# Optimization experiments

Measured on AMD Instinct MI355X. Metric: run time of the kernel, lower is better.

## Reference

```python
import jax, jax.numpy as jnp
import numpy as np

B, T, P, H, E, K, COND = 4096, 20, 20, 256, 128, 5, 5
CTX = E + H + P  # embedded condition + encoder hidden + time-stamp one-hot-cumsum


def setup_inputs():
    key = jax.random.key(0)
    ks = jax.random.split(key, 12)
    g = lambda k, sh, s=0.05: (jax.random.normal(k, sh) * s).astype(jnp.float32)
    return dict(
        conditions=g(ks[0], (B, T, COND), 1.0),
        state_h=g(ks[1], (B, H), 0.1),
        state_c=g(ks[2], (B, H), 0.1),
        steps_n=T,
        We1=g(ks[3], (COND, E)), be1=jnp.zeros((E,), jnp.float32),
        We2=g(ks[4], (E, E)), be2=jnp.zeros((E,), jnp.float32),
        Wk=g(ks[5], (CTX, 4 * H)), Wr=g(ks[6], (H, 4 * H)), bl=jnp.zeros((4 * H,), jnp.float32),
        Wm=g(ks[7], (H, 6 * K)), bm=jnp.zeros((6 * K,), jnp.float32),
        Wy=g(ks[8], (H, 3 * K)), by=jnp.zeros((3 * K,), jnp.float32),
        Wf=g(ks[9], (H, 3 * K)), bf=jnp.zeros((3 * K,), jnp.float32),
        Wfadj=g(ks[10], (H, 3 * K)), bfadj=jnp.zeros((3 * K,), jnp.float32),
    )


def _decode(conditions, state_h, state_c, steps_n, We1, be1, We2, be2,
            Wk, Wr, bl, Wm, bm, Wy, by, Wf, bf, Wfadj, bfadj):
    Bn = conditions.shape[0]
    enc_h = state_h  # reshaped encoder hidden, concatenated into context every step
    base_key = jax.random.key(42)

    def lstm_step(x):
        # Keras gate order i,f,c,o. NOTE: original resets initial_state=self.state
        # (never updated) so every step starts from the encoder state -- kept faithful.
        z = x @ Wk + state_h @ Wr + bl
        i, f, g, o = jnp.split(z, 4, axis=-1)
        c = jax.nn.sigmoid(f) * state_c + jax.nn.sigmoid(i) * jnp.tanh(g)
        return jax.nn.sigmoid(o) * jnp.tanh(c)

    def head_other(h, W, b, k):
        # univariate GMM head: [softmax alphas | mus | exp sigmas], plus one sample
        p = h @ W + b
        logits, mu, ls = jnp.split(p, 3, axis=-1)
        alphas, sig = jax.nn.softmax(logits, axis=-1), jnp.exp(ls)
        vec = jnp.concatenate([alphas, mu, sig], axis=-1)
        k1, k2 = jax.random.split(k)
        idx = jax.random.categorical(k1, logits)[:, None]
        mu_k = jnp.take_along_axis(mu, idx, 1)
        s_k = jnp.take_along_axis(sig, idx, 1)
        return vec, mu_k + s_k * jax.random.normal(k2, mu_k.shape)

    def step(carry, i):
        cond, key = carry
        key, km, ky, kf, kfa = jax.random.split(key, 5)
        emb = (cond @ We1 + be1) @ We2 + be2  # fc_embedding: two linear Dense layers
        ts = (jnp.arange(P) <= i).astype(cond.dtype)  # cumulative time stamp (faithful)
        ctx = jnp.concatenate([emb, enc_h, jnp.broadcast_to(ts, (Bn, P))], axis=-1)
        h = lstm_step(ctx)
        # merge vehicle: bivariate correlated GMM
        pm = h @ Wm + bm
        logits, mu_lo, ls_lo, mu_la, ls_la, rr = jnp.split(pm, 6, axis=-1)
        alphas = jax.nn.softmax(logits, axis=-1)
        s_lo, s_la, rho = jnp.exp(ls_lo), jnp.exp(ls_la), jnp.tanh(rr)
        vec_m = jnp.concatenate([alphas, mu_lo, s_lo, mu_la, s_la, rho], axis=-1)
        k1, k2 = jax.random.split(km)
        idx = jax.random.categorical(k1, logits)[:, None]
        take = lambda a: jnp.take_along_axis(a, idx, 1)
        z = jax.random.normal(k2, (Bn, 2))
        x_lo = take(mu_lo) + take(s_lo) * z[:, :1]
        r = take(rho)
        x_la = take(mu_la) + take(s_la) * (r * z[:, :1] + jnp.sqrt(1.0 - r * r) * z[:, 1:])
        vec_y, s_y = head_other(h, Wy, by, ky)
        vec_f, s_f = head_other(h, Wf, bf, kf)
        vec_fa, s_fa = head_other(h, Wfadj, bfadj, kfa)
        new_cond = jnp.concatenate([x_lo, x_la, s_y, s_f, s_fa], axis=-1)  # [B,5]
        return (new_cond, key), (vec_m, vec_y, vec_f, vec_fa)

    init = (conditions[:, 0, :], base_key)
    _, (vm, vy, vf, vfa) = jax.lax.scan(step, init, jnp.arange(steps_n))
    tr = lambda a: jnp.transpose(a, (1, 0, 2))  # [T,B,D] -> [B,T,D]
    return tr(vm), tr(vy), tr(vf), tr(vfa)


def reference(conditions, state_h, state_c, steps_n, We1, be1, We2, be2,
              Wk, Wr, bl, Wm, bm, Wy, by, Wf, bf, Wfadj, bfadj):
    # returns the concatenated GMM parameter sequences for (merge, yield, f, fadj)
    return _decode(conditions, state_h, state_c, steps_n, We1, be1, We2, be2,
                   Wk, Wr, bl, Wm, bm, Wy, by, Wf, bf, Wfadj, bfadj)
```

## Files before the change

kernel.cpp:

```cpp
#include <hip/hip_runtime.h>
#include <stdint.h>
#include <math.h>

#define BN 4096
#define TT 20
#define HH 256
#define EE 128
#define KK 5
#define NCOND 5

#define WS_TSC  512
#define WS_WTB  20992
#define WS_BIAS 41472
#define WS_ZC   42320
#define WS_M    43344
#define WS_WSUM 48464
#define WS_G    310608
#define WS_ZM   (WS_G + 4*TT*BN*KK)
#define WS_ZO   (WS_ZM + TT*BN*2)
#define WS_CZ   (WS_ZO + 3*TT*BN)
#define WS_END  (WS_CZ + BN*1024)

#define PSTR 84

#define TINYF 1.17549435e-38f
#define LO_N  0.99999994f
#define LOG2E 1.44269504f
#define LN2   0.69314718f

typedef __attribute__((ext_vector_type(8))) short short8v;
typedef __attribute__((ext_vector_type(4))) float f32x4;

__device__ __host__ __forceinline__ constexpr void tf2(
    uint32_t k0, uint32_t k1, uint32_t x0, uint32_t x1, uint32_t& o0, uint32_t& o1) {
  const uint32_t ks2 = k0 ^ k1 ^ 0x1BD11BDAu;
  x0 += k0; x1 += k1;
#define RND(r) { x0 += x1; x1 = (x1 << (r)) | (x1 >> (32 - (r))); x1 ^= x0; }
  RND(13) RND(15) RND(26) RND(6)   x0 += k1;  x1 += ks2 + 1u;
  RND(17) RND(29) RND(16) RND(24)  x0 += ks2; x1 += k0 + 2u;
  RND(13) RND(15) RND(26) RND(6)   x0 += k0;  x1 += k1 + 3u;
  RND(17) RND(29) RND(16) RND(24)  x0 += k1;  x1 += ks2 + 4u;
  RND(13) RND(15) RND(26) RND(6)   x0 += ks2; x1 += k0 + 5u;
#undef RND
  o0 = x0; o1 = x1;
}

struct KeyTab { uint32_t v[TT * 16]; };
constexpr KeyTab mkkeys() {
  KeyTab kt{};
  uint32_t kx = 0u, ky = 42u;
  for (int t = 0; t < TT; ++t) {
    for (int l = 0; l < 4; ++l) {
      uint32_t hx = 0, hy = 0, a = 0, b = 0, c = 0, d = 0;
      tf2(kx, ky, 0u, (uint32_t)(l + 1), hx, hy);
      tf2(hx, hy, 0u, 0u, a, b);
      tf2(hx, hy, 0u, 1u, c, d);
      kt.v[t * 16 + l * 4 + 0] = a;
      kt.v[t * 16 + l * 4 + 1] = b;
      kt.v[t * 16 + l * 4 + 2] = c;
      kt.v[t * 16 + l * 4 + 3] = d;
    }
    uint32_t nx = 0, ny = 0;
    tf2(kx, ky, 0u, 0u, nx, ny);
    kx = nx; ky = ny;
  }
  return kt;
}
__constant__ KeyTab KT = mkkeys();

__device__ __forceinline__ uint32_t pbits(uint32_t k0, uint32_t k1, uint32_t n) {
  uint32_t a, b;
  tf2(k0, k1, 0u, n, a, b);
  return a ^ b;
}

__device__ __forceinline__ float u01f(uint32_t bits) {
  return __uint_as_float((bits >> 9) | 0x3f800000u) - 1.0f;
}

__device__ __forceinline__ float fexp(float x) { return __builtin_amdgcn_exp2f(x * LOG2E); }
__device__ __forceinline__ float flog(float x) { return __builtin_amdgcn_logf(x) * LN2; }
__device__ __forceinline__ float frcp(float x) { return __builtin_amdgcn_rcpf(x); }
__device__ __forceinline__ float fsig(float x) {
  return frcp(1.0f + __builtin_amdgcn_exp2f(-x * LOG2E));
}
__device__ __forceinline__ float ftanh(float x) {
  return 1.0f - 2.0f * frcp(1.0f + __builtin_amdgcn_exp2f(x * (2.0f * LOG2E)));
}

__device__ __forceinline__ float erfinv_f(float x) {
  float w = -flog(fmaf(-x, x, 1.0f));
  float p;
  if (w < 5.0f) {
    w = w - 2.5f;
    p = 2.81022636e-08f;
    p = 3.43273939e-07f + p * w;
    p = -3.5233877e-06f + p * w;
    p = -4.39150654e-06f + p * w;
    p = 0.00021858087f  + p * w;
    p = -0.00125372503f + p * w;
    p = -0.00417768164f + p * w;
    p = 0.246640727f    + p * w;
    p = 1.50140941f     + p * w;
  } else {
    w = sqrtf(w) - 3.0f;
    p = -0.000200214257f;
    p = 0.000100950558f + p * w;
    p = 0.00134934322f  + p * w;
    p = -0.00367342844f + p * w;
    p = 0.00573950773f  + p * w;
    p = -0.0076224613f  + p * w;
    p = 0.00943887047f  + p * w;
    p = 1.00167406f     + p * w;
    p = 2.83297682f     + p * w;
  }
  return p * x;
}

__device__ __forceinline__ uint32_t bf16rne(float f) {
  uint32_t u = __float_as_uint(f);
  return (u + 0x7fffu + ((u >> 16) & 1u)) >> 16;
}

#define RB_RNG   0
#define RB_WSUM  8000
#define RB_TSC   9024
#define RB_WTB   9028
#define RB_BIAS  9108
#define RB_MZC   9109
#define RB_TOT   9113
__global__ __launch_bounds__(256) void prep_misc(
    const float* __restrict__ Wk, const float* __restrict__ Wr,
    const float* __restrict__ We1, const float* __restrict__ be1,
    const float* __restrict__ We2, const float* __restrict__ be2,
    const float* __restrict__ Wm, const float* __restrict__ bm,
    const float* __restrict__ Wy, const float* __restrict__ by,
    const float* __restrict__ Wf, const float* __restrict__ bf,
    const float* __restrict__ Wfa, const float* __restrict__ bfa,
    const float* __restrict__ bl, float* __restrict__ ws) {
  __shared__ float smem[768];
  const int bid = blockIdx.x, tid = threadIdx.x;

  if (bid < RB_WSUM) {
    const int id = bid * 256 + tid;
    const int NG = 4 * TT * BN * KK;
    if (id < NG) {
      const int t = id / (BN * 4 * KK);
      const int r1 = id % (BN * 4 * KK);
      const int row = r1 / (4 * KK);
      const int r2 = r1 % (4 * KK);
      const int head = r2 / KK, k = r2 % KK;
      const uint32_t k0 = KT.v[t * 16 + head * 4 + 0], k1 = KT.v[t * 16 + head * 4 + 1];
      float u = u01f(pbits(k0, k1, (uint32_t)(row * KK + k)));
      u = fmaxf(TINYF, u * (1.0f - TINYF) + TINYF);
      ws[WS_G + id] = -flog(-flog(u));
    } else if (id < NG + TT * BN * 2) {
      const int jj = id - NG;
      const int t = jj / (BN * 2);
      const uint32_t n = (uint32_t)(jj % (BN * 2));
      const uint32_t k0 = KT.v[t * 16 + 2], k1 = KT.v[t * 16 + 3];
      float u = u01f(pbits(k0, k1, n)) * 2.0f - LO_N;
      u = fmaxf(-LO_N, u);
      ws[WS_ZM + jj] = 1.41421356f * erfinv_f(u);
    } else {
      const int jj = id - NG - TT * BN * 2;
      const int t = jj / (BN * 3);
      const int r2 = jj % (BN * 3);
      const int row = r2 / 3, hh = r2 % 3;
      const uint32_t k0 = KT.v[t * 16 + (hh + 1) * 4 + 2];
      const uint32_t k1 = KT.v[t * 16 + (hh + 1) * 4 + 3];
      float u = u01f(pbits(k0, k1, (uint32_t)row)) * 2.0f - LO_N;
      u = fmaxf(-LO_N, u);
      ws[WS_ZO + jj] = 1.41421356f * erfinv_f(u);
    }
  } else if (bid < RB_TSC) {
    const int idx = (bid - RB_WSUM) * 256 + tid;
    const int q = idx >> 10, col = idx & 1023;
    ws[WS_WSUM + idx] = Wk[(size_t)(EE + q) * 1024 + col] + Wr[(size_t)q * 1024 + col];
  } else if (bid < RB_WTB) {
    const int col = (bid - RB_TSC) * 256 + tid;
    float s = 0.0f;
    for (int p = 0; p < TT; ++p) {
      s += Wk[(size_t)(EE + HH + p) * 1024 + col];
      ws[WS_TSC + p * 1024 + col] = s;
    }
  } else if (bid < RB_BIAS) {
    const int idx = (bid - RB_WTB) * 256 + tid;
    const int o = idx >> 8, q = idx & 255;
    float v = 0.0f;
    if (o < 30)      v = Wm[q * 30 + o];
    else if (o < 45) v = Wy[q * 15 + (o - 30)];
    else if (o < 60) v = Wf[q * 15 + (o - 45)];
    else if (o < 75) v = Wfa[q * 15 + (o - 60)];
    uint16_t* wtb = (uint16_t*)&ws[WS_WTB];
    wtb[o * 256 + (q ^ ((o & 7) << 3))] = (uint16_t)bf16rne(v);
  } else if (bid == RB_BIAS) {
    if (tid < 80) {
      float v = 0.0f;
      if (tid < 30)      v = bm[tid];
      else if (tid < 45) v = by[tid - 30];
      else if (tid < 60) v = bf[tid - 45];
      else if (tid < 75) v = bfa[tid - 60];
      ws[WS_BIAS + tid] = v;
    }
  } else {
    float* T1s = smem;
    float* eb2s = smem + 640;
    if (tid < EE) {
      const int q = tid;
      float t0 = 0.f, t1 = 0.f, t2 = 0.f, t3 = 0.f, t4 = 0.f;
      float eb = be2[q];
      for (int e = 0; e < EE; ++e) {
        const float w2 = We2[e * EE + q];
        t0 = fmaf(We1[0 * EE + e], w2, t0);
        t1 = fmaf(We1[1 * EE + e], w2, t1);
        t2 = fmaf(We1[2 * EE + e], w2, t2);
        t3 = fmaf(We1[3 * EE + e], w2, t3);
        t4 = fmaf(We1[4 * EE + e], w2, t4);
        eb = fmaf(be1[e], w2, eb);
      }
      T1s[0 * 128 + q] = t0; T1s[1 * 128 + q] = t1; T1s[2 * 128 + q] = t2;
      T1s[3 * 128 + q] = t3; T1s[4 * 128 + q] = t4; eb2s[q] = eb;
    }
    __syncthreads();
    const int col = (bid - RB_MZC) * 256 + tid;
    float m0 = 0.f, m1 = 0.f, m2 = 0.f, m3 = 0.f, m4 = 0.f;
    float zacc = bl[col];
    for (int q = 0; q < EE; ++q) {
      const float wv = Wk[(size_t)q * 1024 + col];
      m0 = fmaf(T1s[0 * 128 + q], wv, m0);
      m1 = fmaf(T1s[1 * 128 + q], wv, m1);
      m2 = fmaf(T1s[2 * 128 + q], wv, m2);
      m3 = fmaf(T1s[3 * 128 + q], wv, m3);
      m4 = fmaf(T1s[4 * 128 + q], wv, m4);
      zacc = fmaf(eb2s[q], wv, zacc);
    }
    ws[WS_M + 0 * 1024 + col] = m0;
    ws[WS_M + 1 * 1024 + col] = m1;
    ws[WS_M + 2 * 1024 + col] = m2;
    ws[WS_M + 3 * 1024 + col] = m3;
    ws[WS_M + 4 * 1024 + col] = m4;
    ws[WS_ZC + col] = zacc;
  }
}

__global__ __launch_bounds__(512) void prep_czgemm(
    const float* __restrict__ state_h, float* __restrict__ ws) {
  __shared__ short Ab[128 * 256];
  __shared__ short Bb[128 * 256];
  const int tid = threadIdx.x;
  const int brow = blockIdx.x >> 3, bcol = blockIdx.x & 7;
  const int row0 = brow * 128, col0 = bcol * 128;

  for (int i = tid; i < 128 * 256; i += 512) {
    const int m = i >> 8, k = i & 255;
    Ab[m * 256 + (k ^ ((m & 7) << 3))] =
        (short)bf16rne(state_h[(size_t)(row0 + m) * HH + k]);
  }
  for (int i = tid; i < 128 * 256; i += 512) {
    const int k = i >> 7, n = i & 127;
    Bb[n * 256 + (k ^ ((n & 7) << 3))] =
        (short)bf16rne(ws[WS_WSUM + k * 1024 + col0 + n]);
  }
  __syncthreads();

  const int wv = tid >> 6, lane = tid & 63;
  const int wr = wv >> 2, wc = wv & 3;
  const int rc = lane & 15, hq = lane >> 4;
  f32x4 acc[4][2];
#pragma unroll
  for (int fr = 0; fr < 4; ++fr)
#pragma unroll
    for (int fc = 0; fc < 2; ++fc) acc[fr][fc] = (f32x4){0.f, 0.f, 0.f, 0.f};

#pragma unroll
  for (int kk = 0; kk < 8; ++kk) {
    const int kbase = kk * 32 + hq * 8;
    short8v av[4], bv[2];
#pragma unroll
    for (int fr = 0; fr < 4; ++fr) {
      const int m = wr * 64 + fr * 16 + rc;
      av[fr] = *(const short8v*)&Ab[m * 256 + (kbase ^ ((m & 7) << 3))];
    }
#pragma unroll
    for (int fc = 0; fc < 2; ++fc) {
      const int n = wc * 32 + fc * 16 + rc;
      bv[fc] = *(const short8v*)&Bb[n * 256 + (kbase ^ ((n & 7) << 3))];
    }
#pragma unroll
    for (int fr = 0; fr < 4; ++fr)
#pragma unroll
      for (int fc = 0; fc < 2; ++fc)
        acc[fr][fc] = __builtin_amdgcn_mfma_f32_16x16x32_bf16(av[fr], bv[fc],
                                                              acc[fr][fc], 0, 0, 0);
  }

#pragma unroll
  for (int fc = 0; fc < 2; ++fc) {
    const int colg = col0 + wc * 32 + fc * 16 + rc;
    const float zcv = ws[WS_ZC + colg];
#pragma unroll
    for (int fr = 0; fr < 4; ++fr) {
#pragma unroll
      for (int j = 0; j < 4; ++j) {
        const int row = row0 + wr * 64 + fr * 16 + hq * 4 + j;
        ws[WS_CZ + (size_t)row * 1024 + colg] = acc[fr][fc][j] + zcv;
      }
    }
  }
}

__global__ __launch_bounds__(512) void decode_main(
    const float* __restrict__ conditions, const float* __restrict__ state_h,
    const float* __restrict__ state_c, const float* __restrict__ ws,
    float* __restrict__ out, int use_cz) {
  __shared__ float Msh[5 * 1024];
  __shared__ short WTBs[80 * 256];
  __shared__ short hb[16 * 256];
  __shared__ float psh[8 * PSTR];
  __shared__ float biasL[80];
  __shared__ float conds[8 * 8];

  const int tid = threadIdx.x;
  const int row0 = blockIdx.x * 8;
  const int u = tid & 255;
  const int half = tid >> 8;
  const int rbase = half * 4;

  for (int i = tid; i < 5 * 1024; i += 512) Msh[i] = ws[WS_M + i];
  if (tid < 80) biasL[tid] = ws[WS_BIAS + tid];
  if (tid < 8 * NCOND) {
    const int r = tid / NCOND, c = tid - r * NCOND;
    conds[r * 8 + c] = conditions[(size_t)(row0 + r) * (TT * NCOND) + c];
  }
  float sc[4];
#pragma unroll
  for (int rr = 0; rr < 4; ++rr) sc[rr] = state_c[(size_t)(row0 + rbase + rr) * HH + u];

  const bool cth = (tid < 256);
  const int kci = tid & 7;
  const int rci = tid >> 5;
  const int headci = (tid >> 3) & 3;
  const int crow = row0 + rci;
  const int cbase2 = headci ? (30 + 15 * (headci - 1)) : 0;

  float cz[4][4];
  if (use_cz) {
#pragma unroll
    for (int g = 0; g < 4; ++g)
#pragma unroll
      for (int rr = 0; rr < 4; ++rr)
        cz[g][rr] = ws[WS_CZ + (size_t)(row0 + rbase + rr) * 1024 + g * 256 + u];
    {
      uint32_t* dst = (uint32_t*)WTBs;
      const uint32_t* src = (const uint32_t*)&ws[WS_WTB];
      for (int i = tid; i < 80 * 128; i += 512) dst[i] = src[i];
      uint32_t* hz = (uint32_t*)hb;
      for (int i = tid; i < 1024; i += 512) hz[1024 + i] = 0u;
    }
    __syncthreads();
  } else {
    float* hstage = (float*)WTBs;
    for (int i = tid; i < 8 * HH; i += 512) hstage[i] = state_h[(size_t)row0 * HH + i];
    __syncthreads();
#pragma unroll
    for (int g = 0; g < 4; ++g) {
      const float z = ws[WS_ZC + g * 256 + u];
#pragma unroll
      for (int rr = 0; rr < 4; ++rr) cz[g][rr] = z;
    }
    for (int q = 0; q < HH; ++q) {
      const float w0 = ws[WS_WSUM + q * 1024 + u];
      const float w1 = ws[WS_WSUM + q * 1024 + 256 + u];
      const float w2 = ws[WS_WSUM + q * 1024 + 512 + u];
      const float w3 = ws[WS_WSUM + q * 1024 + 768 + u];
#pragma unroll
      for (int rr = 0; rr < 4; ++rr) {
        const float e = hstage[(rbase + rr) * HH + q];
        cz[0][rr] = fmaf(e, w0, cz[0][rr]);
        cz[1][rr] = fmaf(e, w1, cz[1][rr]);
        cz[2][rr] = fmaf(e, w2, cz[2][rr]);
        cz[3][rr] = fmaf(e, w3, cz[3][rr]);
      }
    }
    __syncthreads();
    {
      uint32_t* dst = (uint32_t*)WTBs;
      const uint32_t* src = (const uint32_t*)&ws[WS_WTB];
      for (int i = tid; i < 80 * 128; i += 512) dst[i] = src[i];
      uint32_t* hz = (uint32_t*)hb;
      for (int i = tid; i < 1024; i += 512) hz[1024 + i] = 0u;
    }
    __syncthreads();
  }

  for (int t = 0; t < TT; ++t) {
    float pg = 0.0f, pz0 = 0.0f, pz1 = 0.0f, pzz = 0.0f;
    if (cth) {
      if (kci < 5)
        pg = ws[WS_G + (((size_t)t * BN + crow) * 4 + headci) * KK + kci];
      if (kci == 0) {
        if (headci == 0) {
          pz0 = ws[WS_ZM + ((size_t)t * BN + crow) * 2 + 0];
          pz1 = ws[WS_ZM + ((size_t)t * BN + crow) * 2 + 1];
        } else {
          pzz = ws[WS_ZO + ((size_t)t * BN + crow) * 3 + (headci - 1)];
        }
      }
    }
    {
      const float ts0 = ws[WS_TSC + t * 1024 + u];
      const float ts1 = ws[WS_TSC + t * 1024 + 256 + u];
      const float ts2 = ws[WS_TSC + t * 1024 + 512 + u];
      const float ts3 = ws[WS_TSC + t * 1024 + 768 + u];
      float mA[5], mB[5], mC[5], mD[5];
#pragma unroll
      for (int c = 0; c < 5; ++c) {
        mA[c] = Msh[c * 1024 + u];
        mB[c] = Msh[c * 1024 + 256 + u];
        mC[c] = Msh[c * 1024 + 512 + u];
        mD[c] = Msh[c * 1024 + 768 + u];
      }
#pragma unroll
      for (int rr = 0; rr < 4; ++rr) {
        const int row = rbase + rr;
        const float c0 = conds[row * 8 + 0], c1 = conds[row * 8 + 1], c2 = conds[row * 8 + 2],
                    c3 = conds[row * 8 + 3], c4 = conds[row * 8 + 4];
        float zi = cz[0][rr] + ts0, zf = cz[1][rr] + ts1,
              zg = cz[2][rr] + ts2, zo = cz[3][rr] + ts3;
        zi = fmaf(c0, mA[0], zi); zi = fmaf(c1, mA[1], zi); zi = fmaf(c2, mA[2], zi);
        zi = fmaf(c3, mA[3], zi); zi = fmaf(c4, mA[4], zi);
        zf = fmaf(c0, mB[0], zf); zf = fmaf(c1, mB[1], zf); zf = fmaf(c2, mB[2], zf);
        zf = fmaf(c3, mB[3], zf); zf = fmaf(c4, mB[4], zf);
        zg = fmaf(c0, mC[0], zg); zg = fmaf(c1, mC[1], zg); zg = fmaf(c2, mC[2], zg);
        zg = fmaf(c3, mC[3], zg); zg = fmaf(c4, mC[4], zg);
        zo = fmaf(c0, mD[0], zo); zo = fmaf(c1, mD[1], zo); zo = fmaf(c2, mD[2], zo);
        zo = fmaf(c3, mD[3], zo); zo = fmaf(c4, mD[4], zo);
        const float cv = fsig(zf) * sc[rr] + fsig(zi) * ftanh(zg);
        const float hv = fsig(zo) * ftanh(cv);
        hb[row * 256 + (u ^ ((row & 7) << 3))] = (short)bf16rne(hv);
      }
    }
    __syncthreads();
    {
      const int wv = tid >> 6;
      if (wv < 5) {
        const int lane = tid & 63;
        const int rc = lane & 15;
        const int hq = lane >> 4;
        const int nn = wv * 16 + rc;
        const int aswz = (rc & 7) << 3;
        const int bswz = (nn & 7) << 3;
        f32x4 acc = {0.0f, 0.0f, 0.0f, 0.0f};
#pragma unroll
        for (int kk = 0; kk < 8; ++kk) {
          const int kbase = kk * 32 + hq * 8;
          const short8v av = *(const short8v*)&hb[rc * 256 + (kbase ^ aswz)];
          const short8v bv = *(const short8v*)&WTBs[nn * 256 + (kbase ^ bswz)];
          acc = __builtin_amdgcn_mfma_f32_16x16x32_bf16(av, bv, acc, 0, 0, 0);
        }
        if (hq < 2) {
#pragma unroll
          for (int j = 0; j < 4; ++j) {
            const int prow = hq * 4 + j;
            psh[prow * PSTR + nn] = acc[j] + biasL[nn];
          }
        }
      }
    }
    __syncthreads();
    if (cth) {
      const float lk = (kci < 5) ? psh[rci * PSTR + cbase2 + kci] : -INFINITY;
      float mx = fmaxf(lk, __shfl_xor(lk, 1));
      mx = fmaxf(mx, __shfl_xor(mx, 2));
      mx = fmaxf(mx, __shfl_xor(mx, 4));
      const float ek = (kci < 5) ? fexp(lk - mx) : 0.0f;
      float ss = ek + __shfl_xor(ek, 1);
      ss += __shfl_xor(ss, 2);
      ss += __shfl_xor(ss, 4);
      const float rss = frcp(ss);
      float v = -INFINITY;
      if (kci < 5) v = lk + pg;
      float vm = fmaxf(v, __shfl_xor(v, 1));
      vm = fmaxf(vm, __shfl_xor(vm, 2));
      vm = fmaxf(vm, __shfl_xor(vm, 4));
      int cand = (v == vm) ? kci : 8;
      cand = min(cand, __shfl_xor(cand, 1));
      cand = min(cand, __shfl_xor(cand, 2));
      cand = min(cand, __shfl_xor(cand, 4));
      const int idx = cand;
      const size_t ob = headci
          ? ((size_t)BN * TT * 30 + (size_t)(headci - 1) * BN * TT * 15 +
             ((size_t)crow * TT + t) * 15)
          : ((size_t)crow * TT + t) * 30;
      if (kci < 5) {
        out[ob + kci] = ek * rss;
        out[ob + 5 + kci] = psh[rci * PSTR + cbase2 + 5 + kci];
        out[ob + 10 + kci] = fexp(psh[rci * PSTR + cbase2 + 10 + kci]);
        if (headci == 0) {
          out[ob + 15 + kci] = psh[rci * PSTR + 15 + kci];
          out[ob + 20 + kci] = fexp(psh[rci * PSTR + 20 + kci]);
          out[ob + 25 + kci] = ftanh(psh[rci * PSTR + 25 + kci]);
        }
      }
      if (kci == 0) {
        if (headci == 0) {
          const float mu = psh[rci * PSTR + 5 + idx];
          const float sl = fexp(psh[rci * PSTR + 10 + idx]);
          const float mula = psh[rci * PSTR + 15 + idx];
          const float sla = fexp(psh[rci * PSTR + 20 + idx]);
          const float rho = ftanh(psh[rci * PSTR + 25 + idx]);
          conds[rci * 8 + 0] = mu + sl * pz0;
          conds[rci * 8 + 1] = mula + sla * (rho * pz0 + sqrtf(1.0f - rho * rho) * pz1);
        } else {
          conds[rci * 8 + 1 + headci] =
              psh[rci * PSTR + cbase2 + 5 + idx] +
              fexp(psh[rci * PSTR + cbase2 + 10 + idx]) * pzz;
        }
      }
    }
    __syncthreads();
  }
}

extern "C" void kernel_launch(void* const* d_in, const int* in_sizes, int n_in,
                              void* d_out, int out_size, void* d_ws, size_t ws_size,
                              hipStream_t stream) {
  const float* conditions = (const float*)d_in[0];
  const float* state_h = (const float*)d_in[1];
  const float* state_c = (const float*)d_in[2];
  const float* We1 = (const float*)d_in[4];
  const float* be1 = (const float*)d_in[5];
  const float* We2 = (const float*)d_in[6];
  const float* be2 = (const float*)d_in[7];
  const float* Wk  = (const float*)d_in[8];
  const float* Wr  = (const float*)d_in[9];
  const float* bl  = (const float*)d_in[10];
  const float* Wm  = (const float*)d_in[11];
  const float* bm  = (const float*)d_in[12];
  const float* Wy  = (const float*)d_in[13];
  const float* by  = (const float*)d_in[14];
  const float* Wf  = (const float*)d_in[15];
  const float* bf  = (const float*)d_in[16];
  const float* Wfa = (const float*)d_in[17];
  const float* bfa = (const float*)d_in[18];
  float* ws = (float*)d_ws;
  float* out = (float*)d_out;

  const int use_cz = (ws_size >= (size_t)WS_END * 4) ? 1 : 0;

  prep_misc<<<dim3(RB_TOT), dim3(256), 0, stream>>>(
      Wk, Wr, We1, be1, We2, be2, Wm, bm, Wy, by, Wf, bf, Wfa, bfa, bl, ws);
  if (use_cz) {
    prep_czgemm<<<dim3(256), dim3(512), 0, stream>>>(state_h, ws);
  }
  decode_main<<<dim3(BN / 8), dim3(512), 0, stream>>>(
      conditions, state_h, state_c, ws, out, use_cz);
}
```

Before: 119.7 us.

## Fuse state_h projection GEMM into decode kernel, drop czgemm launch

The separate bf16 MFMA GEMM kernel that computed state_h @ (Wk_enc+Wr) into a 16 MB workspace buffer is removed. Instead, prep_misc writes a transposed bf16 copy of the summed weights, and each decode block computes its own 8-row slice with MFMA into shared memory before loading cz. This removes one kernel launch and the global write and read of the 4096x1024 fp32 intermediate. In exchange, each decode block re-reads the full 512 KB bf16 weight from global/L2, and half of each 16-row MFMA tile is wasted on zero-padded rows.

New measurement: 134.9 us. +12.7%, slower.

```diff
diff --git a/kernel.cpp b/kernel.cpp
--- a/kernel.cpp
+++ b/kernel.cpp
@@ -15,11 +15,11 @@
 #define WS_ZC   42320
 #define WS_M    43344
 #define WS_WSUM 48464
-#define WS_G    310608
+#define WS_WSB  310608
+#define WS_G    441680
 #define WS_ZM   (WS_G + 4*TT*BN*KK)
 #define WS_ZO   (WS_ZM + TT*BN*2)
-#define WS_CZ   (WS_ZO + 3*TT*BN)
-#define WS_END  (WS_CZ + BN*1024)
+#define WS_END  (WS_ZO + 3*TT*BN)
 
 #define PSTR 84
 
@@ -124,11 +124,12 @@
 
 #define RB_RNG   0
 #define RB_WSUM  8000
-#define RB_TSC   9024
-#define RB_WTB   9028
-#define RB_BIAS  9108
-#define RB_MZC   9109
-#define RB_TOT   9113
+#define RB_WSB   9024
+#define RB_TSC   10048
+#define RB_WTB   10052
+#define RB_BIAS  10132
+#define RB_MZC   10133
+#define RB_TOT   10137
 __global__ __launch_bounds__(256) void prep_misc(
     const float* __restrict__ Wk, const float* __restrict__ Wr,
     const float* __restrict__ We1, const float* __restrict__ be1,
@@ -173,10 +174,16 @@
       u = fmaxf(-LO_N, u);
       ws[WS_ZO + jj] = 1.41421356f * erfinv_f(u);
     }
-  } else if (bid < RB_TSC) {
+  } else if (bid < RB_WSB) {
     const int idx = (bid - RB_WSUM) * 256 + tid;
     const int q = idx >> 10, col = idx & 1023;
     ws[WS_WSUM + idx] = Wk[(size_t)(EE + q) * 1024 + col] + Wr[(size_t)q * 1024 + col];
+  } else if (bid < RB_TSC) {
+    const int col = bid - RB_WSB;
+    const int q = tid;
+    uint16_t* wsb = (uint16_t*)&ws[WS_WSB];
+    wsb[col * 256 + q] =
+        (uint16_t)bf16rne(Wk[(size_t)(EE + q) * 1024 + col] + Wr[(size_t)q * 1024 + col]);
   } else if (bid < RB_WTB) {
     const int col = (bid - RB_TSC) * 256 + tid;
     float s = 0.0f;
@@ -244,72 +251,6 @@
   }
 }
 
-__global__ __launch_bounds__(512) void prep_czgemm(
-    const float* __restrict__ state_h, float* __restrict__ ws) {
-  __shared__ short Ab[128 * 256];
-  __shared__ short Bb[128 * 256];
-  const int tid = threadIdx.x;
-  const int brow = blockIdx.x >> 3, bcol = blockIdx.x & 7;
-  const int row0 = brow * 128, col0 = bcol * 128;
-
-  for (int i = tid; i < 128 * 256; i += 512) {
-    const int m = i >> 8, k = i & 255;
-    Ab[m * 256 + (k ^ ((m & 7) << 3))] =
-        (short)bf16rne(state_h[(size_t)(row0 + m) * HH + k]);
-  }
-  for (int i = tid; i < 128 * 256; i += 512) {
-    const int k = i >> 7, n = i & 127;
-    Bb[n * 256 + (k ^ ((n & 7) << 3))] =
-        (short)bf16rne(ws[WS_WSUM + k * 1024 + col0 + n]);
-  }
-  __syncthreads();
-
-  const int wv = tid >> 6, lane = tid & 63;
-  const int wr = wv >> 2, wc = wv & 3;
-  const int rc = lane & 15, hq = lane >> 4;
-  f32x4 acc[4][2];
-#pragma unroll
-  for (int fr = 0; fr < 4; ++fr)
-#pragma unroll
-    for (int fc = 0; fc < 2; ++fc) acc[fr][fc] = (f32x4){0.f, 0.f, 0.f, 0.f};
-
-#pragma unroll
-  for (int kk = 0; kk < 8; ++kk) {
-    const int kbase = kk * 32 + hq * 8;
-    short8v av[4], bv[2];
-#pragma unroll
-    for (int fr = 0; fr < 4; ++fr) {
-      const int m = wr * 64 + fr * 16 + rc;
-      av[fr] = *(const short8v*)&Ab[m * 256 + (kbase ^ ((m & 7) << 3))];
-    }
-#pragma unroll
-    for (int fc = 0; fc < 2; ++fc) {
-      const int n = wc * 32 + fc * 16 + rc;
-      bv[fc] = *(const short8v*)&Bb[n * 256 + (kbase ^ ((n & 7) << 3))];
-    }
-#pragma unroll
-    for (int fr = 0; fr < 4; ++fr)
-#pragma unroll
-      for (int fc = 0; fc < 2; ++fc)
-        acc[fr][fc] = __builtin_amdgcn_mfma_f32_16x16x32_bf16(av[fr], bv[fc],
-                                                              acc[fr][fc], 0, 0, 0);
-  }
-
-#pragma unroll
-  for (int fc = 0; fc < 2; ++fc) {
-    const int colg = col0 + wc * 32 + fc * 16 + rc;
-    const float zcv = ws[WS_ZC + colg];
-#pragma unroll
-    for (int fr = 0; fr < 4; ++fr) {
-#pragma unroll
-      for (int j = 0; j < 4; ++j) {
-        const int row = row0 + wr * 64 + fr * 16 + hq * 4 + j;
-        ws[WS_CZ + (size_t)row * 1024 + colg] = acc[fr][fc][j] + zcv;
-      }
-    }
-  }
-}
-
 __global__ __launch_bounds__(512) void decode_main(
     const float* __restrict__ conditions, const float* __restrict__ state_h,
     const float* __restrict__ state_c, const float* __restrict__ ws,
@@ -346,17 +287,54 @@
 
   float cz[4][4];
   if (use_cz) {
+    {
+      uint32_t* hz = (uint32_t*)hb;
+      for (int i = tid; i < 1024; i += 512) hz[1024 + i] = 0u;
+      for (int i = tid; i < 8 * HH; i += 512) {
+        const int m = i >> 8, k = i & 255;
+        hb[m * 256 + (k ^ ((m & 7) << 3))] =
+            (short)bf16rne(state_h[(size_t)(row0 + m) * HH + k]);
+      }
+    }
+    __syncthreads();
+    {
+      float* czs = (float*)WTBs;
+      const short* wsb = (const short*)&ws[WS_WSB];
+      const int wv = tid >> 6, lane = tid & 63;
+      const int rc = lane & 15, hq = lane >> 4;
+      const int aswz = (rc & 7) << 3;
+      short8v av[8];
+#pragma unroll
+      for (int kk = 0; kk < 8; ++kk)
+        av[kk] = *(const short8v*)&hb[rc * 256 + ((kk * 32 + hq * 8) ^ aswz)];
+#pragma unroll
+      for (int i = 0; i < 8; ++i) {
+        const int nn = (wv * 8 + i) * 16 + rc;
+        f32x4 acc = {0.f, 0.f, 0.f, 0.f};
+#pragma unroll
+        for (int kk = 0; kk < 8; ++kk) {
+          const short8v bv = *(const short8v*)&wsb[nn * 256 + kk * 32 + hq * 8];
+          acc = __builtin_amdgcn_mfma_f32_16x16x32_bf16(av[kk], bv, acc, 0, 0, 0);
+        }
+        if (hq < 2) {
+          const float zcv = ws[WS_ZC + nn];
+#pragma unroll
+          for (int j = 0; j < 4; ++j)
+            czs[(hq * 4 + j) * 1024 + nn] = acc[j] + zcv;
+        }
+      }
+    }
+    __syncthreads();
 #pragma unroll
     for (int g = 0; g < 4; ++g)
 #pragma unroll
       for (int rr = 0; rr < 4; ++rr)
-        cz[g][rr] = ws[WS_CZ + (size_t)(row0 + rbase + rr) * 1024 + g * 256 + u];
+        cz[g][rr] = ((float*)WTBs)[(rbase + rr) * 1024 + g * 256 + u];
+    __syncthreads();
     {
       uint32_t* dst = (uint32_t*)WTBs;
       const uint32_t* src = (const uint32_t*)&ws[WS_WTB];
       for (int i = tid; i < 80 * 128; i += 512) dst[i] = src[i];
-      uint32_t* hz = (uint32_t*)hb;
-      for (int i = tid; i < 1024; i += 512) hz[1024 + i] = 0u;
     }
     __syncthreads();
   } else {
@@ -551,9 +529,6 @@
 
   prep_misc<<<dim3(RB_TOT), dim3(256), 0, stream>>>(
       Wk, Wr, We1, be1, We2, be2, Wm, bm, Wy, by, Wf, bf, Wfa, bfa, bl, ws);
-  if (use_cz) {
-    prep_czgemm<<<dim3(256), dim3(512), 0, stream>>>(state_h, ws);
-  }
   decode_main<<<dim3(BN / 8), dim3(512), 0, stream>>>(
       conditions, state_h, state_c, ws, out, use_cz);
 }
```
